# Performance work log

Hardware: AMD Instinct MI355X
Metric: run time of the kernel (lower is better)

Reference implementation:

```python
import jax, jax.numpy as jnp
import numpy as np

TRIANGLE_TABLE = np.array([
    [-1,-1,-1,-1,-1,-1],[1,0,2,-1,-1,-1],[4,0,3,-1,-1,-1],[1,4,2,1,3,4],
    [3,1,5,-1,-1,-1],[2,3,0,2,5,3],[1,4,0,1,5,4],[4,2,5,-1,-1,-1],
    [4,5,2,-1,-1,-1],[4,1,0,4,5,1],[3,2,0,3,5,2],[1,3,5,-1,-1,-1],
    [4,1,2,4,3,1],[3,0,4,-1,-1,-1],[2,0,1,-1,-1,-1],[-1,-1,-1,-1,-1,-1]], dtype=np.int32)
NUM_TRI_TABLE = np.array([0,1,1,2,1,2,2,1,1,2,2,1,2,1,1,0], dtype=np.int32)
BASE_TET_EDGES = np.array([0,1,0,2,0,3,1,2,1,3,2,3], dtype=np.int32)

NV = 200_000
NT = 800_000

def setup_inputs() -> dict:
    key = jax.random.key(0)
    k1, k2, k3 = jax.random.split(key, 3)
    pos_nx3 = jax.random.normal(k1, (NV, 3), dtype=jnp.float32)
    sdf_n = jax.random.normal(k2, (NV,), dtype=jnp.float32)
    tet_fx4 = jax.random.randint(k3, (NT, 4), 0, NV, dtype=jnp.int32)
    return {"pos_nx3": pos_nx3, "sdf_n": sdf_n, "tet_fx4": tet_fx4}

def map_uv(face_gidx, max_idx):
    # Faithful port of DMTet.map_uv: one 2-triangle UV quad per (potential) tet.
    N = int(np.ceil(np.sqrt((max_idx + 1) // 2)))
    lin = jnp.linspace(0.0, 1.0 - 1.0 / N, N, dtype=jnp.float32)
    tex_y, tex_x = jnp.meshgrid(lin, lin, indexing='ij')
    pad = 0.9 / N
    uvs = jnp.stack([tex_x, tex_y, tex_x + pad, tex_y,
                     tex_x + pad, tex_y + pad, tex_x, tex_y + pad], axis=-1).reshape(-1, 2)
    t = face_gidx // 2
    tet_idx = (t // N) * N + (t % N)   # identity for t < N*N, kept faithful
    tri_idx = face_gidx % 2
    uv_idx = jnp.stack([tet_idx * 4, tet_idx * 4 + tri_idx + 1, tet_idx * 4 + tri_idx + 2], axis=-1)
    return uvs, uv_idx.reshape(-1, 3)

def reference(pos_nx3, sdf_n, tet_fx4):
    # NOTE: marching-tets output sizes are data dependent -> eager (non-jit) jax,
    # matching the torch.unique / boolean-mask structure of the original.
    tri_table = jnp.asarray(TRIANGLE_TABLE)
    num_tri_table = jnp.asarray(NUM_TRI_TABLE)
    base_edges = jnp.asarray(BASE_TET_EDGES)

    occ_n = sdf_n > 0                                   # [Nv]
    occ_fx4 = occ_n[tet_fx4]                            # [T,4]
    occ_sum = occ_fx4.sum(-1)
    valid_tets = (occ_sum > 0) & (occ_sum < 4)

    tet_valid = tet_fx4[valid_tets]                     # [Tv,4]
    all_edges = tet_valid[:, base_edges].reshape(-1, 2) # [Tv*6,2]
    all_edges = jnp.sort(all_edges, axis=1)             # == sort_edges
    unique_edges, idx_map = jnp.unique(all_edges, axis=0, return_inverse=True)

    mask_edges = occ_n[unique_edges].sum(-1) == 1       # sign-crossing edges
    mapping = jnp.where(mask_edges, jnp.cumsum(mask_edges) - 1, -1)
    idx_map = mapping[idx_map.reshape(-1)].reshape(-1, 6)
    interp_v = unique_edges[mask_edges]                 # [Ne,2]

    # linear interpolation of crossing point along each edge
    p = pos_nx3[interp_v]                               # [Ne,2,3]
    s = sdf_n[interp_v] * jnp.array([1.0, -1.0], dtype=sdf_n.dtype)  # negate 2nd sdf
    denom = s.sum(1, keepdims=True)                     # [Ne,1]
    w = s[:, ::-1] / denom                              # flip + normalize
    verts = (p * w[:, :, None]).sum(1)                  # [Ne,3]

    v_id = jnp.array([1, 2, 4, 8], dtype=jnp.int32)
    tetindex = (occ_fx4[valid_tets].astype(jnp.int32) * v_id).sum(-1)  # [Tv]
    num_triangles = num_tri_table[tetindex]
    m1 = num_triangles == 1
    m2 = num_triangles == 2
    f1 = jnp.take_along_axis(idx_map[m1], tri_table[tetindex[m1]][:, :3], axis=1).reshape(-1, 3)
    f2 = jnp.take_along_axis(idx_map[m2], tri_table[tetindex[m2]][:, :6], axis=1).reshape(-1, 3)
    faces = jnp.concatenate([f1, f2], axis=0)

    num_tets = tet_fx4.shape[0]
    tet_gidx = jnp.arange(num_tets, dtype=jnp.int32)[valid_tets]
    face_gidx = jnp.concatenate([
        tet_gidx[m1] * 2,
        jnp.stack([tet_gidx[m2] * 2, tet_gidx[m2] * 2 + 1], axis=-1).reshape(-1)], axis=0)

    uvs, uv_idx = map_uv(face_gidx, num_tets * 2)
    return verts, faces, uvs, uv_idx
```

## Files before the change

### kernel.cpp

```cpp
#include <hip/hip_runtime.h>
#include <cstdio>
#include <cstdint>

typedef unsigned long long u64;

static const int kNV = 200000;
static const int kNT = 800000;
static const int kNUV = 895;
#define UVS_ROWS   3204100LL
#define UVS_FLOATS 6408200LL
#define CAP 3300000

#define NH 392
#define TILE_T 2048
#define BINW 256
#define NBIN 782
#define SUBSH 15
#define FINEB 2048

__device__ const int c_tri[16][6] = {
    {-1,-1,-1,-1,-1,-1},{1,0,2,-1,-1,-1},{4,0,3,-1,-1,-1},{1,4,2,1,3,4},
    {3,1,5,-1,-1,-1},{2,3,0,2,5,3},{1,4,0,1,5,4},{4,2,5,-1,-1,-1},
    {4,5,2,-1,-1,-1},{4,1,0,4,5,1},{3,2,0,3,5,2},{1,3,5,-1,-1,-1},
    {4,1,2,4,3,1},{3,0,4,-1,-1,-1},{2,0,1,-1,-1,-1},{-1,-1,-1,-1,-1,-1}};
__device__ const int c_ntri[16]   = {0,1,1,2,1,2,2,1,1,2,2,1,2,1,1,0};
__device__ const int c_ncross[16] = {0,3,3,4,3,4,4,3,3,4,4,3,4,3,3,0};
__device__ const int c_edges[12] = {0,1,0,2,0,3,1,2,1,3,2,3};

#define PK(m1,m2,nc) (((u64)(m1) << 44) | ((u64)(m2) << 24) | (u64)(nc))

#define SCAN_B 256
#define SCAN_I 8
#define SCAN_TILE (SCAN_B*SCAN_I)

template<typename T>
__global__ void k_scan_partial(const T* __restrict__ in, T* __restrict__ partials, int n){
  __shared__ T sm[SCAN_B];
  int b = blockIdx.x;
  long long base = (long long)b*SCAN_TILE;
  T sum = 0;
  for (int i = threadIdx.x; i < SCAN_TILE; i += SCAN_B){
    long long idx = base + i;
    if (idx < n) sum += in[idx];
  }
  sm[threadIdx.x] = sum; __syncthreads();
  for (int s = SCAN_B/2; s > 0; s >>= 1){
    if ((int)threadIdx.x < s) sm[threadIdx.x] += sm[threadIdx.x + s];
    __syncthreads();
  }
  if (threadIdx.x == 0) partials[b] = sm[0];
}

template<typename T>
__global__ void k_scan_blocksums(T* __restrict__ partials, int nb, T* __restrict__ total_out){
  __shared__ T sm[SCAN_B];
  T carry = 0;
  for (int base = 0; base < nb; base += SCAN_B){
    int i = base + (int)threadIdx.x;
    T v = (i < nb) ? partials[i] : (T)0;
    sm[threadIdx.x] = v; __syncthreads();
    for (int off = 1; off < SCAN_B; off <<= 1){
      T t = ((int)threadIdx.x >= off) ? sm[threadIdx.x - off] : (T)0;
      __syncthreads();
      sm[threadIdx.x] += t;
      __syncthreads();
    }
    if (i < nb) partials[i] = carry + sm[threadIdx.x] - v;
    T tilesum = sm[SCAN_B-1];
    __syncthreads();
    carry += tilesum;
  }
  if (threadIdx.x == 0 && total_out) *total_out = carry;
}

template<typename T>
__global__ void k_scan_apply(const T* __restrict__ in, T* __restrict__ out,
                             const T* __restrict__ partials, int n){
  __shared__ T sm[SCAN_B];
  int b = blockIdx.x;
  long long base = (long long)b*SCAN_TILE + (long long)threadIdx.x*SCAN_I;
  T v[SCAN_I]; T s = 0;
  #pragma unroll
  for (int k = 0; k < SCAN_I; k++){ long long idx = base + k; v[k] = (idx < n) ? in[idx] : (T)0; s += v[k]; }
  sm[threadIdx.x] = s; __syncthreads();
  for (int off = 1; off < 256; off <<= 1){
    T t = ((int)threadIdx.x >= off) ? sm[threadIdx.x - off] : (T)0;
    __syncthreads();
    sm[threadIdx.x] += t;
    __syncthreads();
  }
  T excl = sm[threadIdx.x] - s + partials[b];
  #pragma unroll
  for (int k = 0; k < SCAN_I; k++){ long long idx = base + k; if (idx < n) out[idx] = excl; excl += v[k]; }
}

template<typename T>
static void run_scan(const T* in, T* out, int n, T* partials, hipStream_t s){
  int nb = (n + SCAN_TILE - 1) / SCAN_TILE;
  k_scan_partial<T><<<nb, SCAN_B, 0, s>>>(in, partials, n);
  k_scan_blocksums<T><<<1, SCAN_B, 0, s>>>(partials, nb, out + n);
  k_scan_apply<T><<<nb, SCAN_B, 0, s>>>(in, out, partials, n);
}


__global__ void k_classify_hist(const int* __restrict__ tet, const float* __restrict__ sdf,
                                int* __restrict__ tetinfo, u64* __restrict__ pk,
                                int* __restrict__ blockHist){
  __shared__ int h[NBIN];
  int blk = blockIdx.x;
  for (int j = threadIdx.x; j < NBIN; j += 256) h[j] = 0;
  __syncthreads();
  int t0 = blk*TILE_T;
  for (int k = 0; k < TILE_T/256; k++){
    int t = t0 + k*256 + threadIdx.x;
    if (t < kNT){
      int4 v4 = ((const int4*)tet)[t];
      int pat = ((sdf[v4.x] > 0.0f) ? 1 : 0) | ((sdf[v4.y] > 0.0f) ? 2 : 0)
              | ((sdf[v4.z] > 0.0f) ? 4 : 0) | ((sdf[v4.w] > 0.0f) ? 8 : 0);
      tetinfo[t] = pat;
      int nt_ = c_ntri[pat];
      pk[t] = PK(nt_ == 1, nt_ == 2, c_ncross[pat]);
      if (pat != 0 && pat != 15){
        int vv[4] = {v4.x, v4.y, v4.z, v4.w};
        #pragma unroll
        for (int e = 0; e < 6; e++){
          int i0 = c_edges[2*e], i1 = c_edges[2*e+1];
          if (((pat >> i0) & 1) != ((pat >> i1) & 1)){
            int a = vv[i0], b = vv[i1]; if (a > b){ int tm = a; a = b; b = tm; }
            atomicAdd(&h[a >> 8], 1);
          }
        }
      }
    }
  }
  __syncthreads();
  for (int j = threadIdx.x; j < NBIN; j += 256) blockHist[j*NH + blk] = h[j];
}

__global__ void k_scatter(const int* __restrict__ tet, const int* __restrict__ tetinfo,
                          const u64* __restrict__ psum, const int* __restrict__ bhScan,
                          u64* __restrict__ ebin){
  __shared__ int c[NBIN];
  int blk = blockIdx.x;
  for (int j = threadIdx.x; j < NBIN; j += 256) c[j] = bhScan[j*NH + blk];
  __syncthreads();
  int t0 = blk*TILE_T;
  for (int k = 0; k < TILE_T/256; k++){
    int t = t0 + k*256 + threadIdx.x;
    if (t < kNT){
      int pat = tetinfo[t];
      if (pat != 0 && pat != 15){
        int4 v4 = ((const int4*)tet)[t];
        int vv[4] = {v4.x, v4.y, v4.z, v4.w};
        int seq = (int)(psum[t] & 0xFFFFFF);
        #pragma unroll
        for (int e = 0; e < 6; e++){
          int i0 = c_edges[2*e], i1 = c_edges[2*e+1];
          if (((pat >> i0) & 1) != ((pat >> i1) & 1)){
            int a = vv[i0], b = vv[i1]; if (a > b){ int tm = a; a = b; b = tm; }
            int pos = atomicAdd(&c[a >> 8], 1);
            ebin[pos] = ((u64)(unsigned)a << 40) | ((u64)(unsigned)b << 22) | (unsigned)seq;
            seq++;
          }
        }
      }
    }
  }
}

__global__ void k_fine(const int* __restrict__ bhScan, const u64* __restrict__ ebin,
                       u64* __restrict__ efin){
  __shared__ int h[FINEB];
  __shared__ int ss[256];
  int bin = blockIdx.x;
  int binStart = bhScan[bin*NH];
  int binEnd   = bhScan[(bin+1)*NH];
  int a0 = bin << 8;
  for (int j = threadIdx.x; j < FINEB; j += 256) h[j] = 0;
  __syncthreads();
  for (int i = binStart + threadIdx.x; i < binEnd; i += 256){
    u64 p = ebin[i];
    int a = (int)(p >> 40);
    int bh = (int)((p >> 22) & 0x3FFFF) >> SUBSH;
    atomicAdd(&h[((a - a0) << 3) | bh], 1);
  }
  __syncthreads();
  int tid = threadIdx.x;
  int base8 = tid*8;
  int loc[8]; int s = 0;
  #pragma unroll
  for (int q = 0; q < 8; q++){ loc[q] = h[base8+q]; s += loc[q]; }
  ss[tid] = s; __syncthreads();
  for (int off = 1; off < 256; off <<= 1){
    int v = (tid >= off) ? ss[tid - off] : 0;
    __syncthreads();
    ss[tid] += v;
    __syncthreads();
  }
  int excl = ss[tid] - s;
  #pragma unroll
  for (int q = 0; q < 8; q++){ h[base8+q] = excl; excl += loc[q]; }
  __syncthreads();
  for (int i = binStart + tid; i < binEnd; i += 256){
    u64 p = ebin[i];
    int a = (int)(p >> 40);
    int bh = (int)((p >> 22) & 0x3FFFF) >> SUBSH;
    int pos = binStart + atomicAdd(&h[((a - a0) << 3) | bh], 1);
    efin[pos] = p;
  }
}

#define FB 256
#define FH 32
#define FW (FB + 2*FH)
__global__ void k_flags(const u64* __restrict__ efin, const int* __restrict__ totp,
                        int* __restrict__ firstI, unsigned* __restrict__ meta){
  __shared__ u64 ld[FW];
  __shared__ unsigned char fl[FW];
  int total = *totp;
  int tid = threadIdx.x;
  long long base = (long long)blockIdx.x * FB;
  long long gi = base + tid;
  if (base >= total){
    if (gi < CAP){ firstI[gi] = 0; meta[gi] = 0; }
    return;
  }
  for (int x = tid; x < FW; x += FB){
    long long g = base - FH + x;
    ld[x] = (g >= 0 && g < total) ? (efin[g] >> 22) : ~0ULL;
  }
  __syncthreads();
  for (int x = tid; x < FW; x += FB){
    u64 key = ld[x];
    u64 grp = key >> SUBSH;
    unsigned char f = 1;
    for (int y = x-1; y >= 0; y--){
      u64 ky = ld[y];
      if ((ky >> SUBSH) != grp) break;
      if (ky == key){ f = 0; break; }
    }
    fl[x] = f;
  }
  __syncthreads();
  if (gi < total){
    int x = FH + tid;
    u64 key = ld[x];
    u64 grp = key >> SUBSH;
    int sx = x; while (sx > 0 && (ld[sx-1] >> SUBSH) == grp) sx--;
    int ex = x+1; while (ex < FW && (ld[ex] >> SUBSH) == grp) ex++;
    int first, rank, off;
    if (sx > 0 && ex < FW){
      first = fl[x];
      int rk = 0;
      for (int y = sx; y < ex; y++) if (fl[y] && ld[y] < key) rk++;
      rank = rk; off = x - sx;
    } else {
      u64 keyg = efin[gi] >> 22;
      u64 grpg = keyg >> SUBSH;
      long long s = gi; while (s > 0 && ((efin[s-1] >> 22) >> SUBSH) == grpg) s--;
      long long e = gi + 1; while (e < total && ((efin[e] >> 22) >> SUBSH) == grpg) e++;
      int f = 1;
      for (long long j = s; j < gi; j++) if ((efin[j] >> 22) == keyg){ f = 0; break; }
      int rk = 0;
      for (long long j = s; j < e; j++){
        u64 kj = efin[j] >> 22;
        if (kj < keyg){
          bool fj = true;
          for (long long l = s; l < j; l++) if ((efin[l] >> 22) == kj){ fj = false; break; }
          if (fj) rk++;
        }
      }
      first = f; rank = rk; off = (int)(gi - s);
    }
    firstI[gi] = first;
    meta[gi] = (unsigned)rank | ((unsigned)off << 12) | ((unsigned)first << 24);
  } else if (gi < CAP){
    firstI[gi] = 0;
    meta[gi] = 0;
  }
}

__global__ void k_emit(const u64* __restrict__ efin, const int* __restrict__ totp,
                       const int* __restrict__ fscan, const unsigned* __restrict__ meta,
                       const float* __restrict__ pos, const float* __restrict__ sdf,
                       float* __restrict__ out, int* __restrict__ rankBySeq){
  int total = *totp;
  int i = blockIdx.x*256 + threadIdx.x;
  if (i >= total) return;
  u64 p = efin[i];
  unsigned m = meta[i];
  int rank = m & 0xFFF, off = (m >> 12) & 0xFFF, first = (m >> 24) & 1;
  int r = fscan[i - off] + rank;
  rankBySeq[(int)(p & 0x3FFFFF)] = r;
  if (first){
    int a = (int)(p >> 40);
    int b = (int)((p >> 22) & 0x3FFFF);
    float sa = sdf[a], sb = sdf[b];
    float denom = sa - sb;
    float w0 = (-sb) / denom;
    float w1 = sa / denom;
    out[3LL*r + 0] = pos[3*a+0]*w0 + pos[3*b+0]*w1;
    out[3LL*r + 1] = pos[3*a+1]*w0 + pos[3*b+1]*w1;
    out[3LL*r + 2] = pos[3*a+2]*w0 + pos[3*b+2]*w1;
  }
}

__global__ void k_faces(const int* __restrict__ tetinfo, const u64* __restrict__ psum,
                        const int* __restrict__ fscan, const int* __restrict__ rankBySeq,
                        float* __restrict__ out){
  int t = blockIdx.x*256 + threadIdx.x; if (t >= kNT) return;
  int pat = tetinfo[t];
  int nt_ = c_ntri[pat];
  if (nt_ == 0) return;
  u64 tot = psum[kNT];
  int Nm1 = (int)(tot >> 44), Nm2 = (int)((tot >> 24) & 0xFFFFF);
  int Ne = fscan[CAP];
  long long faces_off = 3LL*Ne;
  long long uvidx_off = faces_off + 3LL*((long long)Nm1 + 2LL*Nm2) + UVS_FLOATS;
  u64 ps = psum[t];
  int m1v = (int)(ps >> 44), m2v = (int)((ps >> 24) & 0xFFFFF);
  int seq = (int)(ps & 0xFFFFFF);
  int er[6];
  int j = 0;
  #pragma unroll
  for (int e = 0; e < 6; e++){
    int i0 = c_edges[2*e], i1 = c_edges[2*e+1];
    if (((pat >> i0) & 1) != ((pat >> i1) & 1)){
      er[e] = rankBySeq[seq + j];
      j++;
    } else er[e] = -1;
  }
  for (int k = 0; k < nt_; k++){
    long long row = (nt_ == 1) ? (long long)m1v : ((long long)Nm1 + 2LL*m2v + k);
    #pragma unroll
    for (int c = 0; c < 3; c++){
      int slot = c_tri[pat][3*k + c];
      out[faces_off + 3*row + c] = (float)er[slot];
    }
    out[uvidx_off + 3*row + 0] = (float)(4*t);
    out[uvidx_off + 3*row + 1] = (float)(4*t + k + 1);
    out[uvidx_off + 3*row + 2] = (float)(4*t + k + 2);
  }
}

__global__ void k_uvs(const u64* __restrict__ psum, const int* __restrict__ fscan,
                      float* __restrict__ out){
  long long r = (long long)blockIdx.x*256 + threadIdx.x;
  if (r >= UVS_ROWS) return;
  u64 tot = psum[kNT];
  int Nm1 = (int)(tot >> 44), Nm2 = (int)((tot >> 24) & 0xFFFFF);
  int Ne = fscan[CAP];
  long long off = 3LL*Ne + 3LL*((long long)Nm1 + 2LL*Nm2);
  int cell = (int)(r >> 2), k = (int)(r & 3);
  int iy = cell / kNUV, ix = cell - iy*kNUV;
  const float delta = (1.0f - 1.0f/895.0f) / 894.0f;
  const float pad = 0.9f / 895.0f;
  float x = (float)ix * delta, y = (float)iy * delta;
  float u = x + ((k == 1 || k == 2) ? pad : 0.0f);
  float v = y + ((k >= 2) ? pad : 0.0f);
  out[off + 2*r]     = u;
  out[off + 2*r + 1] = v;
}

static inline int divup(int a, int b){ return (a + b - 1) / b; }

extern "C" void kernel_launch(void* const* d_in, const int* in_sizes, int n_in,
                              void* d_out, int out_size, void* d_ws, size_t ws_size,
                              hipStream_t stream){
  const float* pos = (const float*)d_in[0];
  const float* sdf = (const float*)d_in[1];
  const int*   tet = (const int*)d_in[2];
  float* out = (float*)d_out;

  char* ws = (char*)d_ws;
  size_t off = 0;
  auto alloc = [&](size_t bytes) -> char* {
    char* p = ws + off; off += (bytes + 255) & ~(size_t)255; return p;
  };
  int* tetinfo     = (int*)alloc((size_t)kNT*4);
  u64* pk          = (u64*)alloc((size_t)kNT*8);
  u64* psum        = (u64*)alloc((size_t)(kNT+1)*8);
  int* blockHist   = (int*)alloc((size_t)NBIN*NH*4);
  int* bhScan      = (int*)alloc((size_t)(NBIN*NH+1)*4);
  u64* ebin        = (u64*)alloc((size_t)CAP*8);
  u64* efin        = (u64*)alloc((size_t)CAP*8);
  int* rankBySeq   = (int*)alloc((size_t)CAP*4);
  int* fscan       = (int*)alloc((size_t)(CAP+1)*4);
  u64* part64      = (u64*)alloc(4096*8);
  int* partI       = (int*)alloc(4096*4);
  int* firstI      = (int*)ebin;
  unsigned* meta   = (unsigned*)((char*)ebin + (size_t)CAP*4);
  if (off > ws_size){
    fprintf(stderr, "[dmtet] workspace too small: need %zu have %zu\n", off, ws_size);
    return;
  }

  k_classify_hist<<<NH, 256, 0, stream>>>(tet, sdf, tetinfo, pk, blockHist);
  run_scan<u64>(pk, psum, kNT, part64, stream);
  run_scan<int>(blockHist, bhScan, NBIN*NH, partI, stream);
  k_scatter<<<NH, 256, 0, stream>>>(tet, tetinfo, psum, bhScan, ebin);
  k_fine<<<NBIN, 256, 0, stream>>>(bhScan, ebin, efin);
  k_flags<<<divup(CAP,FB), FB, 0, stream>>>(efin, bhScan + NBIN*NH, firstI, meta);
  run_scan<int>(firstI, fscan, CAP, partI, stream);
  k_emit<<<divup(CAP,256), 256, 0, stream>>>(efin, bhScan + NBIN*NH, fscan, meta,
                                             pos, sdf, out, rankBySeq);
  k_faces<<<divup(kNT,256), 256, 0, stream>>>(tetinfo, psum, fscan, rankBySeq, out);
  k_uvs<<<divup((int)UVS_ROWS,256), 256, 0, stream>>>(psum, fscan, out);
}
```

Before: 225.0 us.

## Replace per-element flag scan with block-count scan and fused in-block rank emission

The separate flags kernel, the full-length three-pass scan over CAP flags and the emit kernel are replaced with a decoupled scheme. A count kernel writes one unique-edge count per 256-element block, a single-block scan turns those into block prefixes, and an emit kernel recomputes first-flags in shared memory and derives ranks with a local prefix. This removes the per-element firstI/meta arrays and the global scan traffic. In exchange the dedup flag pass runs twice, and groups that span block boundaries fall back to slower global-memory walks.

```diff
diff --git a/kernel.cpp b/kernel.cpp
--- a/kernel.cpp
+++ b/kernel.cpp
@@ -17,6 +17,11 @@
 #define NBIN 782
 #define SUBSH 15
 #define FINEB 2048
+
+#define FB 256
+#define FH 32
+#define FW (FB + 2*FH)
+#define NFB ((CAP + FB - 1) / FB)
 
 __device__ const int c_tri[16][6] = {
     {-1,-1,-1,-1,-1,-1},{1,0,2,-1,-1,-1},{4,0,3,-1,-1,-1},{1,4,2,1,3,4},
@@ -83,7 +88,7 @@
   #pragma unroll
   for (int k = 0; k < SCAN_I; k++){ long long idx = base + k; v[k] = (idx < n) ? in[idx] : (T)0; s += v[k]; }
   sm[threadIdx.x] = s; __syncthreads();
-  for (int off = 1; off < 256; off <<= 1){
+  for (int off = 1; off < SCAN_B; off <<= 1){
     T t = ((int)threadIdx.x >= off) ? sm[threadIdx.x - off] : (T)0;
     __syncthreads();
     sm[threadIdx.x] += t;
@@ -210,29 +215,22 @@
   }
 }
 
-#define FB 256
-#define FH 32
-#define FW (FB + 2*FH)
-__global__ void k_flags(const u64* __restrict__ efin, const int* __restrict__ totp,
-                        int* __restrict__ firstI, unsigned* __restrict__ meta){
+__global__ void k_fcount(const u64* __restrict__ efin, const int* __restrict__ totp,
+                         int* __restrict__ blockAgg){
   __shared__ u64 ld[FW];
   __shared__ unsigned char fl[FW];
+  __shared__ int wsum[4];
   int total = *totp;
   int tid = threadIdx.x;
   long long base = (long long)blockIdx.x * FB;
-  long long gi = base + tid;
-  if (base >= total){
-    if (gi < CAP){ firstI[gi] = 0; meta[gi] = 0; }
-    return;
-  }
+  if (base >= total){ if (tid == 0) blockAgg[blockIdx.x] = 0; return; }
   for (int x = tid; x < FW; x += FB){
     long long g = base - FH + x;
     ld[x] = (g >= 0 && g < total) ? (efin[g] >> 22) : ~0ULL;
   }
   __syncthreads();
   for (int x = tid; x < FW; x += FB){
-    u64 key = ld[x];
-    u64 grp = key >> SUBSH;
+    u64 key = ld[x]; u64 grp = key >> SUBSH;
     unsigned char f = 1;
     for (int y = x-1; y >= 0; y--){
       u64 ky = ld[y];
@@ -242,63 +240,114 @@
     fl[x] = f;
   }
   __syncthreads();
+  long long gi = base + tid;
+  int flag = 0;
   if (gi < total){
     int x = FH + tid;
-    u64 key = ld[x];
-    u64 grp = key >> SUBSH;
+    u64 key = ld[x]; u64 grp = key >> SUBSH;
     int sx = x; while (sx > 0 && (ld[sx-1] >> SUBSH) == grp) sx--;
-    int ex = x+1; while (ex < FW && (ld[ex] >> SUBSH) == grp) ex++;
-    int first, rank, off;
-    if (sx > 0 && ex < FW){
-      first = fl[x];
-      int rk = 0;
-      for (int y = sx; y < ex; y++) if (fl[y] && ld[y] < key) rk++;
-      rank = rk; off = x - sx;
-    } else {
-      u64 keyg = efin[gi] >> 22;
-      u64 grpg = keyg >> SUBSH;
-      long long s = gi; while (s > 0 && ((efin[s-1] >> 22) >> SUBSH) == grpg) s--;
-      long long e = gi + 1; while (e < total && ((efin[e] >> 22) >> SUBSH) == grpg) e++;
-      int f = 1;
-      for (long long j = s; j < gi; j++) if ((efin[j] >> 22) == keyg){ f = 0; break; }
-      int rk = 0;
-      for (long long j = s; j < e; j++){
-        u64 kj = efin[j] >> 22;
-        if (kj < keyg){
-          bool fj = true;
-          for (long long l = s; l < j; l++) if ((efin[l] >> 22) == kj){ fj = false; break; }
-          if (fj) rk++;
-        }
+    if (sx > 0) flag = fl[x];
+    else {
+      long long s = gi; while (s > 0 && ((efin[s-1] >> 22) >> SUBSH) == grp) s--;
+      flag = 1;
+      for (long long j = s; j < gi; j++) if ((efin[j] >> 22) == key){ flag = 0; break; }
+    }
+  }
+  unsigned long long bal = __ballot(flag);
+  if ((tid & 63) == 0) wsum[tid >> 6] = __popcll(bal);
+  __syncthreads();
+  if (tid == 0) blockAgg[blockIdx.x] = wsum[0] + wsum[1] + wsum[2] + wsum[3];
+}
+
+__global__ void k_emit2(const u64* __restrict__ efin, const int* __restrict__ totp,
+                        const int* __restrict__ blockPrefix,
+                        const float* __restrict__ pos, const float* __restrict__ sdf,
+                        float* __restrict__ out, int* __restrict__ rankBySeq){
+  __shared__ u64 ld[FW];
+  __shared__ unsigned char fl[FW];
+  __shared__ int fp[FW];
+  __shared__ int ps[FW/2];
+  int total = *totp;
+  int tid = threadIdx.x;
+  long long base = (long long)blockIdx.x * FB;
+  if (base >= total) return;
+  for (int x = tid; x < FW; x += FB){
+    long long g = base - FH + x;
+    ld[x] = (g >= 0 && g < total) ? (efin[g] >> 22) : ~0ULL;
+  }
+  __syncthreads();
+  for (int x = tid; x < FW; x += FB){
+    u64 key = ld[x]; u64 grp = key >> SUBSH;
+    unsigned char f = 1;
+    for (int y = x-1; y >= 0; y--){
+      u64 ky = ld[y];
+      if ((ky >> SUBSH) != grp) break;
+      if (ky == key){ f = 0; break; }
+    }
+    fl[x] = f;
+  }
+  __syncthreads();
+  if (tid < FW/2) ps[tid] = (int)fl[2*tid] + (int)fl[2*tid+1];
+  __syncthreads();
+  for (int off = 1; off < FW/2; off <<= 1){
+    int v = (tid >= off && tid < FW/2) ? ps[tid-off] : 0;
+    __syncthreads();
+    if (tid < FW/2) ps[tid] += v;
+    __syncthreads();
+  }
+  if (tid < FW/2){
+    int a0 = fl[2*tid], a1 = fl[2*tid+1];
+    int excl = ps[tid] - a0 - a1;
+    fp[2*tid] = excl; fp[2*tid+1] = excl + a0;
+  }
+  __syncthreads();
+  long long gi = base + tid;
+  if (gi >= total) return;
+  int blkPref = blockPrefix[blockIdx.x];
+  bool spanL = (base > 0) && ((ld[0] >> SUBSH) == (ld[FH] >> SUBSH));
+  int x = FH + tid;
+  u64 key = ld[x]; u64 grp = key >> SUBSH;
+  int sx = x; while (sx > 0 && (ld[sx-1] >> SUBSH) == grp) sx--;
+  int ex = x+1; while (ex < FW && (ld[ex] >> SUBSH) == grp) ex++;
+  int r, first;
+  if (sx > 0 && ex < FW && !spanL){
+    first = fl[x];
+    int rk = 0;
+    for (int y = sx; y < ex; y++) if (fl[y] && ld[y] < key) rk++;
+    r = blkPref + (fp[sx] - fp[FH]) + rk;
+  } else {
+    long long s = gi; while (s > 0 && ((efin[s-1] >> 22) >> SUBSH) == grp) s--;
+    long long e = gi + 1; while (e < total && ((efin[e] >> 22) >> SUBSH) == grp) e++;
+    first = 1;
+    for (long long j = s; j < gi; j++) if ((efin[j] >> 22) == key){ first = 0; break; }
+    int rk = 0;
+    for (long long j = s; j < e; j++){
+      u64 kj = efin[j] >> 22;
+      if (kj < key){
+        bool fj = true;
+        for (long long l = s; l < j; l++) if ((efin[l] >> 22) == kj){ fj = false; break; }
+        if (fj) rk++;
       }
-      first = f; rank = rk; off = (int)(gi - s);
-    }
-    firstI[gi] = first;
-    meta[gi] = (unsigned)rank | ((unsigned)off << 12) | ((unsigned)first << 24);
-  } else if (gi < CAP){
-    firstI[gi] = 0;
-    meta[gi] = 0;
-  }
-}
-
-__global__ void k_emit(const u64* __restrict__ efin, const int* __restrict__ totp,
-                       const int* __restrict__ fscan, const unsigned* __restrict__ meta,
-                       const float* __restrict__ pos, const float* __restrict__ sdf,
-                       float* __restrict__ out, int* __restrict__ rankBySeq){
-  int total = *totp;
-  int i = blockIdx.x*256 + threadIdx.x;
-  if (i >= total) return;
-  u64 p = efin[i];
-  unsigned m = meta[i];
-  int rank = m & 0xFFF, off = (m >> 12) & 0xFFF, first = (m >> 24) & 1;
-  int r = fscan[i - off] + rank;
+    }
+    long long sb = (s / FB) * FB;
+    int cnt = blockPrefix[(int)(s / FB)];
+    for (long long j = sb; j < s; j++){
+      u64 kj = efin[j] >> 22; u64 gj = kj >> SUBSH;
+      long long gs = j; while (gs > 0 && ((efin[gs-1] >> 22) >> SUBSH) == gj) gs--;
+      bool fj = true;
+      for (long long l = gs; l < j; l++) if ((efin[l] >> 22) == kj){ fj = false; break; }
+      if (fj) cnt++;
+    }
+    r = cnt + rk;
+  }
+  u64 p = efin[gi];
   rankBySeq[(int)(p & 0x3FFFFF)] = r;
   if (first){
     int a = (int)(p >> 40);
     int b = (int)((p >> 22) & 0x3FFFF);
-    float sa = sdf[a], sb = sdf[b];
-    float denom = sa - sb;
-    float w0 = (-sb) / denom;
-    float w1 = sa / denom;
+    float sa = sdf[a], sb2 = sdf[b];
+    float denom = sa - sb2;
+    float w0 = (-sb2) / denom, w1 = sa / denom;
     out[3LL*r + 0] = pos[3*a+0]*w0 + pos[3*b+0]*w1;
     out[3LL*r + 1] = pos[3*a+1]*w0 + pos[3*b+1]*w1;
     out[3LL*r + 2] = pos[3*a+2]*w0 + pos[3*b+2]*w1;
@@ -306,7 +355,7 @@
 }
 
 __global__ void k_faces(const int* __restrict__ tetinfo, const u64* __restrict__ psum,
-                        const int* __restrict__ fscan, const int* __restrict__ rankBySeq,
+                        const int* __restrict__ Nep, const int* __restrict__ rankBySeq,
                         float* __restrict__ out){
   int t = blockIdx.x*256 + threadIdx.x; if (t >= kNT) return;
   int pat = tetinfo[t];
@@ -314,7 +363,7 @@
   if (nt_ == 0) return;
   u64 tot = psum[kNT];
   int Nm1 = (int)(tot >> 44), Nm2 = (int)((tot >> 24) & 0xFFFFF);
-  int Ne = fscan[CAP];
+  int Ne = *Nep;
   long long faces_off = 3LL*Ne;
   long long uvidx_off = faces_off + 3LL*((long long)Nm1 + 2LL*Nm2) + UVS_FLOATS;
   u64 ps = psum[t];
@@ -343,13 +392,13 @@
   }
 }
 
-__global__ void k_uvs(const u64* __restrict__ psum, const int* __restrict__ fscan,
+__global__ void k_uvs(const u64* __restrict__ psum, const int* __restrict__ Nep,
                       float* __restrict__ out){
   long long r = (long long)blockIdx.x*256 + threadIdx.x;
   if (r >= UVS_ROWS) return;
   u64 tot = psum[kNT];
   int Nm1 = (int)(tot >> 44), Nm2 = (int)((tot >> 24) & 0xFFFFF);
-  int Ne = fscan[CAP];
+  int Ne = *Nep;
   long long off = 3LL*Ne + 3LL*((long long)Nm1 + 2LL*Nm2);
   int cell = (int)(r >> 2), k = (int)(r & 3);
   int iy = cell / kNUV, ix = cell - iy*kNUV;
@@ -385,11 +434,9 @@
   u64* ebin        = (u64*)alloc((size_t)CAP*8);
   u64* efin        = (u64*)alloc((size_t)CAP*8);
   int* rankBySeq   = (int*)alloc((size_t)CAP*4);
-  int* fscan       = (int*)alloc((size_t)(CAP+1)*4);
+  int* blockAgg    = (int*)alloc((size_t)(NFB+1)*4);
   u64* part64      = (u64*)alloc(4096*8);
   int* partI       = (int*)alloc(4096*4);
-  int* firstI      = (int*)ebin;
-  unsigned* meta   = (unsigned*)((char*)ebin + (size_t)CAP*4);
   if (off > ws_size){
     fprintf(stderr, "[dmtet] workspace too small: need %zu have %zu\n", off, ws_size);
     return;
@@ -400,10 +447,9 @@
   run_scan<int>(blockHist, bhScan, NBIN*NH, partI, stream);
   k_scatter<<<NH, 256, 0, stream>>>(tet, tetinfo, psum, bhScan, ebin);
   k_fine<<<NBIN, 256, 0, stream>>>(bhScan, ebin, efin);
-  k_flags<<<divup(CAP,FB), FB, 0, stream>>>(efin, bhScan + NBIN*NH, firstI, meta);
-  run_scan<int>(firstI, fscan, CAP, partI, stream);
-  k_emit<<<divup(CAP,256), 256, 0, stream>>>(efin, bhScan + NBIN*NH, fscan, meta,
-                                             pos, sdf, out, rankBySeq);
-  k_faces<<<divup(kNT,256), 256, 0, stream>>>(tetinfo, psum, fscan, rankBySeq, out);
-  k_uvs<<<divup((int)UVS_ROWS,256), 256, 0, stream>>>(psum, fscan, out);
-}
+  k_fcount<<<NFB, FB, 0, stream>>>(efin, bhScan + NBIN*NH, blockAgg);
+  k_scan_blocksums<int><<<1, SCAN_B, 0, stream>>>(blockAgg, NFB, blockAgg + NFB);
+  k_emit2<<<NFB, FB, 0, stream>>>(efin, bhScan + NBIN*NH, blockAgg, pos, sdf, out, rankBySeq);
+  k_faces<<<divup(kNT,256), 256, 0, stream>>>(tetinfo, psum, blockAgg + NFB, rankBySeq, out);
+  k_uvs<<<divup((int)UVS_ROWS,256), 256, 0, stream>>>(psum, blockAgg + NFB, out);
+}
```

Measured after the change: 256.3 us. +13.9%, slower.
